# Kernel optimization log

Measured on AMD Instinct MI355X. Metric: run time of the kernel, lower is better.

Reference implementation:

```python
import jax, jax.numpy as jnp
import numpy as np

PD = 256            # pretrain_dim == dim_in (standard mode)
DZ = 128            # dim_z
PD2 = PD + 2        # feature dim after concatenating 2-d coords
FD = PD + 2 * PD2   # final_dim = 772
TEMP = float(DZ) ** 0.5
EPS = 1e-12
N1, N2 = 4096, 2048


def _lin_init(key, din, dout):
    w = jax.random.normal(key, (dout, din), jnp.float32) * 0.02
    b = jnp.zeros((dout,), jnp.float32)
    return w, b


def _lin(x, w, b):
    return x @ w.T + b


def setup_inputs() -> dict:
    key = jax.random.key(0)
    ks = jax.random.split(key, 13)
    lm_X = jax.random.normal(ks[0], (N1, PD), jnp.float32)
    lm_Y = jax.random.normal(ks[1], (N1, 2), jnp.float32)
    tg_X = jax.random.normal(ks[2], (N2, PD), jnp.float32)
    tg_Y = jax.random.normal(ks[3], (N2, 2), jnp.float32)
    lm_delay = jax.random.uniform(ks[4], (N1,), jnp.float32)
    tg_delay = jax.random.uniform(ks[5], (N2,), jnp.float32)
    aq_w, aq_b = _lin_init(ks[6], PD, DZ)    # att_attribute q proj
    ak_w, ak_b = _lin_init(ks[7], PD, DZ)    # att_attribute k proj
    w1_w, w1_b = _lin_init(ks[8], PD2, PD2)  # self.w_1
    w2_w, w2_b = _lin_init(ks[9], PD2, PD2)  # self.w_2
    pq_w, pq_b = _lin_init(ks[10], FD, DZ)   # pred attention q proj
    pk_w, pk_b = _lin_init(ks[11], PD, DZ)   # pred attention k proj
    pv_w, pv_b = _lin_init(ks[12], 2, 2)     # pred attention v proj
    gamma1 = jnp.ones((1, 1), jnp.float32)
    gamma2 = jnp.ones((1, 1), jnp.float32)
    gamma3 = jnp.ones((1, 1), jnp.float32)
    alpha = jnp.ones((1, 1), jnp.float32)
    beta = jnp.zeros((1, 1), jnp.float32)
    return dict(lm_X=lm_X, lm_Y=lm_Y, tg_X=tg_X, tg_Y=tg_Y,
                lm_delay=lm_delay, tg_delay=tg_delay,
                aq_w=aq_w, aq_b=aq_b, ak_w=ak_w, ak_b=ak_b,
                w1_w=w1_w, w1_b=w1_b, w2_w=w2_w, w2_b=w2_b,
                pq_w=pq_w, pq_b=pq_b, pk_w=pk_w, pk_b=pk_b,
                pv_w=pv_w, pv_b=pv_b,
                gamma1=gamma1, gamma2=gamma2, gamma3=gamma3,
                alpha=alpha, beta=beta)


def reference(lm_X, lm_Y, tg_X, tg_Y, lm_delay, tg_delay,
              aq_w, aq_b, ak_w, ak_b,
              w1_w, w1_b, w2_w, w2_b,
              pq_w, pq_b, pk_w, pk_b, pv_w, pv_b,
              gamma1, gamma2, gamma3, alpha, beta):
    n2 = tg_X.shape[0]
    a = alpha[0, 0]
    b0 = beta[0, 0]

    lm_feature = jnp.concatenate([lm_X, lm_Y], axis=1)            # [N1, PD2]
    tg_feature_0 = jnp.concatenate([tg_X, jnp.zeros((n2, 2), lm_X.dtype)], axis=1)
    router_0 = jnp.mean(lm_feature, axis=0)                        # [PD2]

    delay_score = jnp.exp(-gamma1[0, 0] * (a * lm_delay + b0))     # [N1]
    rou0 = jnp.exp(-gamma2[0, 0] * (a * tg_delay + b0))            # [N2]
    rou1 = jnp.exp(-gamma3[0, 0] * (a * tg_delay + b0))            # [N2]

    # SimpleAttention1: attribute score of targets over landmarks
    q = _lin(tg_X, aq_w, aq_b)
    k = _lin(lm_X, ak_w, ak_b)
    attr = jnp.exp(jax.nn.softmax((q / TEMP) @ k.T, axis=-1))      # [N2, N1]

    # Degree-normalized propagation of adj_matrix_0 (block-structured:
    # lm rows = identity, tg rows = [attr | I | rou0-col], router row = [delay | 0 | 1]).
    deg_tg0 = 1.0 + attr.sum(axis=1) + rou0                        # [N2]
    tg_prop0 = (attr @ lm_feature + tg_feature_0 + rou0[:, None] * router_0[None, :]) \
               / (deg_tg0 + EPS)[:, None]
    router_prop0 = (delay_score @ lm_feature + router_0) / (1.0 + delay_score.sum() + EPS)

    tg_feature_1 = _lin(tg_prop0, w1_w, w1_b)                      # [N2, PD2]
    router_1 = _lin(router_prop0[None, :], w1_w, w1_b)             # [1, PD2]

    # Second propagation: adj_matrix_1 = I + rou1 on tg->router column.
    tg_prop1 = (tg_feature_1 + rou1[:, None] * router_1) / (1.0 + rou1 + EPS)[:, None]
    tg_feature_2 = _lin(tg_prop1, w2_w, w2_b)                      # [N2, PD2]

    final_tg_feature = jnp.concatenate([tg_X, tg_feature_1, tg_feature_2], axis=-1)  # [N2, FD]

    # SimpleAttention2 (collaborative MLP prediction)
    q2 = _lin(final_tg_feature, pq_w, pq_b)
    k2 = _lin(lm_X, pk_w, pk_b)
    v2 = _lin(lm_Y, pv_w, pv_b)
    attn2 = jax.nn.softmax((q2 / TEMP) @ k2.T, axis=-1)            # [N2, N1]
    y_pred = attn2 @ v2                                            # [N2, 2]
    return y_pred, final_tg_feature
```

## Files before the change

kernel.cpp:

```cpp
#include <hip/hip_runtime.h>

#define N1 4096
#define N2 2048
#define PD 256
#define DZ 128
#define PD2 258
#define PD2P 264
#define FD 772
#define FDP 776
#define APN 272
#define APLD 72
#define SPLITS 16

typedef short s8v __attribute__((ext_vector_type(8)));
typedef float f32x4 __attribute__((ext_vector_type(4)));

__device__ __forceinline__ short f2b(float f) {
    union { float f; unsigned u; } v; v.f = f;
    unsigned r = v.u + 0x7fffu + ((v.u >> 16) & 1u);
    return (short)(r >> 16);
}
__device__ __forceinline__ float sb2f(short s) {
    union { unsigned u; float f; } v;
    v.u = ((unsigned)(unsigned short)s) << 16;
    return v.f;
}

constexpr int R0 = N2 * PD;
constexpr int R1 = R0 + PD2 * PD2P;
constexpr int R2 = R1 + PD2 * PD2P;
constexpr int R3 = R2 + DZ * FDP;
constexpr int R4 = R3 + APN * N1;
constexpr int R5 = R4 + 4096;
constexpr int R6 = R5 + 2048;
constexpr int R7 = R6 + N2 * 4;
constexpr int R8 = R7 + N2 * 6;

__global__ __launch_bounds__(256) void cvt_all(
    const float* __restrict__ lmX, const float* __restrict__ lmY,
    const float* __restrict__ tgX,
    const float* __restrict__ pqw, const float* __restrict__ w1w,
    const float* __restrict__ w2w,
    const float* __restrict__ lmd, const float* __restrict__ tgd,
    const float* __restrict__ g1, const float* __restrict__ g2,
    const float* __restrict__ g3, const float* __restrict__ al,
    const float* __restrict__ be,
    const float* __restrict__ pvw, const float* __restrict__ pvb,
    short* __restrict__ w1wb, short* __restrict__ w2wb,
    short* __restrict__ pqwb, short* __restrict__ lmFTb,
    float* __restrict__ dscore, float* __restrict__ rou0,
    float* __restrict__ rou1, float* __restrict__ v2b,
    float* __restrict__ Z, short* __restrict__ finalFb,
    short* __restrict__ tgp1b, float* __restrict__ outF)
{
    int i = blockIdx.x * 256 + threadIdx.x;
    if (i < R0) { int r = i >> 8, c = i & 255;
                  float v = tgX[i];
                  outF[(size_t)r * FD + c] = v;
                  finalFb[(size_t)r * FDP + c] = f2b(v); return; }
    if (i < R1) { int j = i - R0; int r = j / PD2P, c = j - r * PD2P;
                  w1wb[j] = (c < PD2) ? f2b(w1w[r * PD2 + c]) : (short)0; return; }
    if (i < R2) { int j = i - R1; int r = j / PD2P, c = j - r * PD2P;
                  w2wb[j] = (c < PD2) ? f2b(w2w[r * PD2 + c]) : (short)0; return; }
    if (i < R3) { int j = i - R2; int r = j / FDP, c = j - r * FDP;
                  pqwb[j] = (c < FD) ? f2b(pqw[r * FD + c]) : (short)0; return; }
    if (i < R4) { int j = i - R3; int c = j >> 12, r = j & (N1 - 1);
                  float v = 0.f;
                  if (c < PD) v = lmX[(size_t)r * PD + c];
                  else if (c < PD2) v = lmY[r * 2 + (c - PD)];
                  else if (c == PD2) v = 1.0f;
                  lmFTb[j] = f2b(v); return; }
    if (i < R5) { int j = i - R4;
                  float a = al[0], b = be[0];
                  dscore[j] = __expf(-g1[0] * (a * lmd[j] + b));
                  float y0 = lmY[2 * j], y1 = lmY[2 * j + 1];
                  v2b[2 * j]     = pvw[0] * y0 + pvw[1] * y1 + pvb[0];
                  v2b[2 * j + 1] = pvw[2] * y0 + pvw[3] * y1 + pvb[1];
                  if (j < N2) { float t = a * tgd[j] + b;
                                rou0[j] = __expf(-g2[0] * t);
                                rou1[j] = __expf(-g3[0] * t); }
                  return; }
    if (i < R6) { Z[i - R5] = 0.f; return; }
    if (i < R7) { int j = i - R6; int r = j >> 2;
                  finalFb[(size_t)r * FDP + FD + (j & 3)] = 0; return; }
    if (i < R8) { int j = i - R7; int r = j / 6;
                  tgp1b[(size_t)r * PD2P + PD2 + (j - r * 6)] = 0; return; }
}

__global__ __launch_bounds__(256) void rkq_kernel(
    const float* __restrict__ lmX, const float* __restrict__ tgX,
    const float* __restrict__ aqw, const float* __restrict__ aqb,
    const float* __restrict__ akw, const float* __restrict__ akb,
    const float* __restrict__ pkw, const float* __restrict__ pkb,
    const short* __restrict__ lmFTb, const float* __restrict__ dscore,
    float* __restrict__ router0, float* __restrict__ routerp0,
    short* __restrict__ kk, short* __restrict__ qb)
{
    __shared__ __align__(16) short LDS[5120];
    const int j = blockIdx.x, tid = threadIdx.x;
    const int lane = tid & 63, wv = tid >> 6;
    const int wm = wv >> 1, wn = wv & 1;
    const int lm = lane & 15, lq = lane >> 4;
    const f32x4 zero4 = {0.f, 0.f, 0.f, 0.f};

    if (j < 258) {
        float* r1 = (float*)LDS;
        float* r2 = r1 + 256;
        float* r3 = r2 + 256;
        const short* rowp = lmFTb + (size_t)j * N1;
        float s1 = 0.f, s2 = 0.f, s3 = 0.f;
        for (int i = tid; i < N1; i += 256) {
            float v = sb2f(rowp[i]);
            float d = dscore[i];
            s1 += v; s2 += d * v; s3 += d;
        }
        r1[tid] = s1; r2[tid] = s2; r3[tid] = s3; __syncthreads();
        for (int o = 128; o > 0; o >>= 1) {
            if (tid < o) { r1[tid] += r1[tid + o]; r2[tid] += r2[tid + o]; r3[tid] += r3[tid + o]; }
            __syncthreads();
        }
        if (tid == 0) {
            float r0v = r1[0] / (float)N1;
            router0[j] = r0v;
            routerp0[j] = (r2[0] + r0v) / (1.f + r3[0] + 1e-12f);
        }
        return;
    }
    short* Als = LDS;
    short* Bls = LDS + 64 * 40;
    f32x4 acc[2][2] = {{zero4, zero4}, {zero4, zero4}};
    const int r = tid >> 2, cgp = tid & 3;
    if (j < 514) {
        int jt = j - 258;
        int row0 = (jt >> 2) * 64, col0 = (jt & 3) * 64;
        for (int k0 = 0; k0 < 256; k0 += 32) {
            int gk = k0 + cgp * 8;
            const float* ap = lmX + (size_t)(row0 + r) * PD + gk;
            int c = col0 + r;
            const float* bp = (c < 128) ? akw + (size_t)c * PD + gk
                                        : pkw + (size_t)(c - 128) * PD + gk;
            s8v va, vb;
#pragma unroll
            for (int q = 0; q < 8; ++q) { va[q] = f2b(ap[q]); vb[q] = f2b(bp[q]); }
            *(s8v*)(Als + r * 40 + cgp * 8) = va;
            *(s8v*)(Bls + r * 40 + cgp * 8) = vb;
            __syncthreads();
            s8v af[2], bf[2];
#pragma unroll
            for (int mt = 0; mt < 2; ++mt)
                af[mt] = *(const s8v*)(Als + (wm * 32 + mt * 16 + lm) * 40 + lq * 8);
#pragma unroll
            for (int nt = 0; nt < 2; ++nt)
                bf[nt] = *(const s8v*)(Bls + (wn * 32 + nt * 16 + lm) * 40 + lq * 8);
#pragma unroll
            for (int mt = 0; mt < 2; ++mt)
#pragma unroll
                for (int nt = 0; nt < 2; ++nt)
                    acc[mt][nt] = __builtin_amdgcn_mfma_f32_16x16x32_bf16(
                        af[mt], bf[nt], acc[mt][nt], 0, 0, 0);
            __syncthreads();
        }
#pragma unroll
        for (int mt = 0; mt < 2; ++mt)
#pragma unroll
            for (int nt = 0; nt < 2; ++nt) {
                int c = col0 + wn * 32 + nt * 16 + lm;
                float bv = (c < 128) ? akb[c] : pkb[c - 128];
#pragma unroll
                for (int i = 0; i < 4; ++i) {
                    int rr = row0 + wm * 32 + mt * 16 + lq * 4 + i;
                    kk[(size_t)rr * 256 + c] = f2b(acc[mt][nt][i] + bv);
                }
            }
    } else {
        int jt = j - 514;
        int row0 = (jt >> 1) * 64, col0 = (jt & 1) * 64;
        for (int k0 = 0; k0 < 256; k0 += 32) {
            int gk = k0 + cgp * 8;
            const float* ap = tgX + (size_t)(row0 + r) * PD + gk;
            const float* bp = aqw + (size_t)(col0 + r) * PD + gk;
            s8v va, vb;
#pragma unroll
            for (int q = 0; q < 8; ++q) { va[q] = f2b(ap[q]); vb[q] = f2b(bp[q]); }
            *(s8v*)(Als + r * 40 + cgp * 8) = va;
            *(s8v*)(Bls + r * 40 + cgp * 8) = vb;
            __syncthreads();
            s8v af[2], bf[2];
#pragma unroll
            for (int mt = 0; mt < 2; ++mt)
                af[mt] = *(const s8v*)(Als + (wm * 32 + mt * 16 + lm) * 40 + lq * 8);
#pragma unroll
            for (int nt = 0; nt < 2; ++nt)
                bf[nt] = *(const s8v*)(Bls + (wn * 32 + nt * 16 + lm) * 40 + lq * 8);
#pragma unroll
            for (int mt = 0; mt < 2; ++mt)
#pragma unroll
                for (int nt = 0; nt < 2; ++nt)
                    acc[mt][nt] = __builtin_amdgcn_mfma_f32_16x16x32_bf16(
                        af[mt], bf[nt], acc[mt][nt], 0, 0, 0);
            __syncthreads();
        }
        const float INV_TEMP = 0.08838834764831845f;
#pragma unroll
        for (int mt = 0; mt < 2; ++mt)
#pragma unroll
            for (int nt = 0; nt < 2; ++nt) {
                int c = col0 + wn * 32 + nt * 16 + lm;
                float bv = aqb[c];
#pragma unroll
                for (int i = 0; i < 4; ++i) {
                    int rr = row0 + wm * 32 + mt * 16 + lq * 4 + i;
                    qb[(size_t)rr * DZ + c] = f2b(INV_TEMP * (acc[mt][nt][i] + bv));
                }
            }
    }
}

__global__ __launch_bounds__(256) void scores_e(
    const short* __restrict__ Q, const short* __restrict__ Kk,
    short* __restrict__ E, float* __restrict__ Z,
    const float* __restrict__ rp0, const float* __restrict__ w1w,
    const float* __restrict__ w1b, float* __restrict__ router1)
{
    const int j = blockIdx.x, tid = threadIdx.x;
    if (j == 512) {
        for (int c = tid; c < PD2; c += 256) {
            float s = w1b[c];
            const float* wr = w1w + (size_t)c * PD2;
            for (int k = 0; k < PD2; ++k) s += rp0[k] * wr[k];
            router1[c] = s;
        }
        return;
    }
    __shared__ __align__(16) short LDS[10240];
    short* Als = LDS;
    short* Bls = LDS + 128 * 40;
    const int lane = tid & 63, wv = tid >> 6;
    const int wm = wv >> 1, wn = wv & 1;
    const int lm = lane & 15, lq = lane >> 4;
    const int row0 = (j >> 5) * 128, col0 = (j & 31) * 128;
    const f32x4 zero4 = {0.f, 0.f, 0.f, 0.f};
    f32x4 acc[4][4];
#pragma unroll
    for (int mt = 0; mt < 4; ++mt)
#pragma unroll
        for (int nt = 0; nt < 4; ++nt) acc[mt][nt] = zero4;
    for (int k0 = 0; k0 < 128; k0 += 32) {
#pragma unroll
        for (int l = 0; l < 2; ++l) {
            int id = l * 256 + tid;
            int r = id >> 2, cgp = id & 3;
            int gk = k0 + cgp * 8;
            *(s8v*)(Als + r * 40 + cgp * 8) = *(const s8v*)(Q + (size_t)(row0 + r) * DZ + gk);
            *(s8v*)(Bls + r * 40 + cgp * 8) = *(const s8v*)(Kk + (size_t)(col0 + r) * 256 + gk);
        }
        __syncthreads();
        s8v af[4], bf[4];
#pragma unroll
        for (int mt = 0; mt < 4; ++mt)
            af[mt] = *(const s8v*)(Als + (wm * 64 + mt * 16 + lm) * 40 + lq * 8);
#pragma unroll
        for (int nt = 0; nt < 4; ++nt)
            bf[nt] = *(const s8v*)(Bls + (wn * 64 + nt * 16 + lm) * 40 + lq * 8);
#pragma unroll
        for (int mt = 0; mt < 4; ++mt)
#pragma unroll
            for (int nt = 0; nt < 4; ++nt)
                acc[mt][nt] = __builtin_amdgcn_mfma_f32_16x16x32_bf16(
                    af[mt], bf[nt], acc[mt][nt], 0, 0, 0);
        __syncthreads();
    }
#pragma unroll
    for (int mt = 0; mt < 4; ++mt)
#pragma unroll
        for (int i = 0; i < 4; ++i) {
            int r = row0 + wm * 64 + mt * 16 + lq * 4 + i;
            float rs = 0.f;
#pragma unroll
            for (int nt = 0; nt < 4; ++nt) {
                int c = col0 + wn * 64 + nt * 16 + lm;
                float e = __expf(acc[mt][nt][i]);
                E[(size_t)r * N1 + c] = f2b(e);
                rs += e;
            }
#pragma unroll
            for (int msk = 1; msk < 16; msk <<= 1) rs += __shfl_xor(rs, msk, 64);
            if (lm == 0) atomicAdd(&Z[r], rs);
        }
}

__global__ __launch_bounds__(512) void ap_gemm(const short* __restrict__ E,
                                               const float* __restrict__ Z,
                                               const short* __restrict__ lmFTb,
                                               short* __restrict__ part)
{
    __shared__ __align__(16) short LDS[28800];
    const int tid = threadIdx.x, bid = blockIdx.x;
    const int lane = tid & 63, w8 = tid >> 6;
    const int lm = lane & 15, lq = lane >> 4;
    const int s = bid & 15, row0 = (bid >> 4) * 128;
    const int kbase = s * (N1 / SPLITS);
    short* Als = LDS;
    short* Bls = LDS + 128 * APLD;
    const f32x4 zero4 = {0.f, 0.f, 0.f, 0.f};
    f32x4 acc[17];
#pragma unroll
    for (int nt = 0; nt < 17; ++nt) acc[nt] = zero4;
    for (int it = 0; it < (N1 / SPLITS) / 64; ++it) {
        int k0 = kbase + it * 64;
#pragma unroll
        for (int l = 0; l < 2; ++l) {
            int id = l * 512 + tid;
            int r = id >> 3, gg = id & 7;
            s8v ev = *(const s8v*)(E + (size_t)(row0 + r) * N1 + k0 + gg * 8);
            float invZ = __builtin_amdgcn_rcpf(Z[row0 + r]);
            s8v av;
#pragma unroll
            for (int q = 0; q < 8; ++q)
                av[q] = f2b(__expf(sb2f(ev[q]) * invZ));
            *(s8v*)(Als + r * APLD + gg * 8) = av;
        }
#pragma unroll
        for (int l = 0; l < 5; ++l) {
            int id = l * 512 + tid;
            if (id < APN * 8) {
                int r = id >> 3, gg = id & 7;
                *(s8v*)(Bls + r * APLD + gg * 8) =
                    *(const s8v*)(lmFTb + (size_t)r * N1 + k0 + gg * 8);
            }
        }
        __syncthreads();
        s8v a0 = *(const s8v*)(Als + (w8 * 16 + lm) * APLD + lq * 8);
        s8v a1 = *(const s8v*)(Als + (w8 * 16 + lm) * APLD + 32 + lq * 8);
#pragma unroll
        for (int nt = 0; nt < 17; ++nt) {
            s8v b0 = *(const s8v*)(Bls + (nt * 16 + lm) * APLD + lq * 8);
            s8v b1 = *(const s8v*)(Bls + (nt * 16 + lm) * APLD + 32 + lq * 8);
            acc[nt] = __builtin_amdgcn_mfma_f32_16x16x32_bf16(a0, b0, acc[nt], 0, 0, 0);
            acc[nt] = __builtin_amdgcn_mfma_f32_16x16x32_bf16(a1, b1, acc[nt], 0, 0, 0);
        }
        __syncthreads();
    }
    short* op = part + (size_t)s * N2 * APN;
#pragma unroll
    for (int nt = 0; nt < 17; ++nt) {
        int c = nt * 16 + lm;
#pragma unroll
        for (int i = 0; i < 4; ++i) {
            int r = row0 + w8 * 16 + lq * 4 + i;
            op[(size_t)r * APN + c] = f2b(acc[nt][i]);
        }
    }
}

__global__ __launch_bounds__(256) void fix_tgp0(const short* __restrict__ part,
                                                const float* __restrict__ tgX,
                                                const float* __restrict__ rou0,
                                                const float* __restrict__ router0,
                                                short* __restrict__ outb) {
    int r = blockIdx.x;
    int tid = threadIdx.x;
    __shared__ float sAsum;
    float s0 = 0.f, s1 = 0.f;
#pragma unroll
    for (int s = 0; s < SPLITS; ++s)
        s0 += sb2f(part[((size_t)s * N2 + r) * APN + tid]);
    if (tid < 8) {
#pragma unroll
        for (int s = 0; s < SPLITS; ++s)
            s1 += sb2f(part[((size_t)s * N2 + r) * APN + 256 + tid]);
    }
    if (tid == 2) sAsum = s1;
    __syncthreads();
    float ro = rou0[r];
    float inv = 1.f / (1.f + sAsum + ro + 1e-12f);
    {
        float v = (s0 + tgX[(size_t)r * PD + tid] + ro * router0[tid]) * inv;
        outb[(size_t)r * PD2P + tid] = f2b(v);
    }
    if (tid < 8) {
        int c = 256 + tid;
        float v = 0.f;
        if (c < PD2) v = (s1 + ro * router0[c]) * inv;
        outb[(size_t)r * PD2P + c] = f2b(v);
    }
}

__global__ __launch_bounds__(256) void w_gemm(
    const short* __restrict__ A, const short* __restrict__ B,
    const float* __restrict__ bias,
    float* __restrict__ outFcol, short* __restrict__ fFbcol,
    const float* __restrict__ rou1, const float* __restrict__ router1,
    short* __restrict__ tgp1b)
{
    __shared__ __align__(16) short LDS[5120];
    short* Als = LDS;
    short* Bls = LDS + 64 * 40;
    const int tid = threadIdx.x;
    const int lane = tid & 63, wv = tid >> 6;
    const int wm = wv >> 1, wn = wv & 1;
    const int lm = lane & 15, lq = lane >> 4;
    const int row0 = blockIdx.y * 64, col0 = blockIdx.x * 64;
    const f32x4 zero4 = {0.f, 0.f, 0.f, 0.f};
    f32x4 acc[2][2] = {{zero4, zero4}, {zero4, zero4}};
    const s8v zero8 = {0, 0, 0, 0, 0, 0, 0, 0};
    const int r = tid >> 2, cgp = tid & 3;
    for (int k0 = 0; k0 < PD2P; k0 += 32) {
        int gk = k0 + cgp * 8;
        s8v va = zero8, vb = zero8;
        if (gk < PD2P) {
            va = *(const s8v*)(A + (size_t)(row0 + r) * PD2P + gk);
            if (col0 + r < PD2) vb = *(const s8v*)(B + (size_t)(col0 + r) * PD2P + gk);
        }
        *(s8v*)(Als + r * 40 + cgp * 8) = va;
        *(s8v*)(Bls + r * 40 + cgp * 8) = vb;
        __syncthreads();
        s8v af[2], bf[2];
#pragma unroll
        for (int mt = 0; mt < 2; ++mt)
            af[mt] = *(const s8v*)(Als + (wm * 32 + mt * 16 + lm) * 40 + lq * 8);
#pragma unroll
        for (int nt = 0; nt < 2; ++nt)
            bf[nt] = *(const s8v*)(Bls + (wn * 32 + nt * 16 + lm) * 40 + lq * 8);
#pragma unroll
        for (int mt = 0; mt < 2; ++mt)
#pragma unroll
            for (int nt = 0; nt < 2; ++nt)
                acc[mt][nt] = __builtin_amdgcn_mfma_f32_16x16x32_bf16(
                    af[mt], bf[nt], acc[mt][nt], 0, 0, 0);
        __syncthreads();
    }
#pragma unroll
    for (int mt = 0; mt < 2; ++mt)
#pragma unroll
        for (int nt = 0; nt < 2; ++nt) {
            int c = col0 + wn * 32 + nt * 16 + lm;
            if (c >= PD2) continue;
            float bv = bias[c];
            float rc = router1 ? router1[c] : 0.f;
#pragma unroll
            for (int i = 0; i < 4; ++i) {
                int rr = row0 + wm * 32 + mt * 16 + lq * 4 + i;
                float v = acc[mt][nt][i] + bv;
                outFcol[(size_t)rr * FD + c] = v;
                fFbcol[(size_t)rr * FDP + c] = f2b(v);
                if (tgp1b) {
                    float ro = rou1[rr];
                    tgp1b[(size_t)rr * PD2P + c] =
                        f2b((v + ro * rc) / (1.f + ro + 1e-12f));
                }
            }
        }
}

__global__ __launch_bounds__(256) void q2_gemm(
    const short* __restrict__ A, const short* __restrict__ B,
    const float* __restrict__ bias, short* __restrict__ outB)
{
    __shared__ __align__(16) short LDS[5120];
    short* Als = LDS;
    short* Bls = LDS + 64 * 40;
    const int tid = threadIdx.x;
    const int lane = tid & 63, wv = tid >> 6;
    const int wm = wv >> 1, wn = wv & 1;
    const int lm = lane & 15, lq = lane >> 4;
    const int row0 = blockIdx.y * 64, col0 = blockIdx.x * 64;
    const f32x4 zero4 = {0.f, 0.f, 0.f, 0.f};
    f32x4 acc[2][2] = {{zero4, zero4}, {zero4, zero4}};
    const s8v zero8 = {0, 0, 0, 0, 0, 0, 0, 0};
    const int r = tid >> 2, cgp = tid & 3;
    for (int k0 = 0; k0 < FDP; k0 += 32) {
        int gk = k0 + cgp * 8;
        s8v va = zero8, vb = zero8;
        if (gk < FDP) {
            va = *(const s8v*)(A + (size_t)(row0 + r) * FDP + gk);
            vb = *(const s8v*)(B + (size_t)(col0 + r) * FDP + gk);
        }
        *(s8v*)(Als + r * 40 + cgp * 8) = va;
        *(s8v*)(Bls + r * 40 + cgp * 8) = vb;
        __syncthreads();
        s8v af[2], bf[2];
#pragma unroll
        for (int mt = 0; mt < 2; ++mt)
            af[mt] = *(const s8v*)(Als + (wm * 32 + mt * 16 + lm) * 40 + lq * 8);
#pragma unroll
        for (int nt = 0; nt < 2; ++nt)
            bf[nt] = *(const s8v*)(Bls + (wn * 32 + nt * 16 + lm) * 40 + lq * 8);
#pragma unroll
        for (int mt = 0; mt < 2; ++mt)
#pragma unroll
            for (int nt = 0; nt < 2; ++nt)
                acc[mt][nt] = __builtin_amdgcn_mfma_f32_16x16x32_bf16(
                    af[mt], bf[nt], acc[mt][nt], 0, 0, 0);
        __syncthreads();
    }
    const float INV_TEMP = 0.08838834764831845f;
#pragma unroll
    for (int mt = 0; mt < 2; ++mt)
#pragma unroll
        for (int nt = 0; nt < 2; ++nt) {
            int c = col0 + wn * 32 + nt * 16 + lm;
            float bv = bias[c];
#pragma unroll
            for (int i = 0; i < 4; ++i) {
                int rr = row0 + wm * 32 + mt * 16 + lq * 4 + i;
                outB[(size_t)rr * DZ + c] = f2b(INV_TEMP * (acc[mt][nt][i] + bv));
            }
        }
}

__global__ __launch_bounds__(256) void attn2_flash(
    const short* __restrict__ Q, const short* __restrict__ Kk,
    const float* __restrict__ V, float* __restrict__ part2)
{
    __shared__ __align__(16) short Qls[64 * 136];
    __shared__ __align__(16) short Kls[64 * 136];
    __shared__ float Vls[128];
    const int tid = threadIdx.x;
    const int lane = tid & 63, wv = tid >> 6;
    const int lm = lane & 15, lq = lane >> 4;
    const int chunk = blockIdx.x & 15, row0 = (blockIdx.x >> 4) * 64;
    const f32x4 zero4 = {0.f, 0.f, 0.f, 0.f};
#pragma unroll
    for (int l = 0; l < 4; ++l) {
        int id = l * 256 + tid;
        int r = id >> 4, g = id & 15;
        *(s8v*)(Qls + r * 136 + g * 8) = *(const s8v*)(Q + (size_t)(row0 + r) * DZ + g * 8);
    }
    __syncthreads();
    s8v af[4];
#pragma unroll
    for (int ks = 0; ks < 4; ++ks)
        af[ks] = *(const s8v*)(Qls + (wv * 16 + lm) * 136 + ks * 32 + lq * 8);
    float z[4] = {0.f, 0.f, 0.f, 0.f};
    float y0[4] = {0.f, 0.f, 0.f, 0.f};
    float y1[4] = {0.f, 0.f, 0.f, 0.f};
    for (int t = 0; t < 4; ++t) {
        int col0 = chunk * 256 + t * 64;
        __syncthreads();
#pragma unroll
        for (int l = 0; l < 4; ++l) {
            int id = l * 256 + tid;
            int r = id >> 4, g = id & 15;
            *(s8v*)(Kls + r * 136 + g * 8) =
                *(const s8v*)(Kk + (size_t)(col0 + r) * 256 + 128 + g * 8);
        }
        if (tid < 128) Vls[tid] = V[col0 * 2 + tid];
        __syncthreads();
        f32x4 acc[4];
#pragma unroll
        for (int nt = 0; nt < 4; ++nt) acc[nt] = zero4;
#pragma unroll
        for (int nt = 0; nt < 4; ++nt)
#pragma unroll
            for (int ks = 0; ks < 4; ++ks) {
                s8v bf = *(const s8v*)(Kls + (nt * 16 + lm) * 136 + ks * 32 + lq * 8);
                acc[nt] = __builtin_amdgcn_mfma_f32_16x16x32_bf16(af[ks], bf, acc[nt], 0, 0, 0);
            }
        float v0[4], v1[4];
#pragma unroll
        for (int nt = 0; nt < 4; ++nt) {
            v0[nt] = Vls[(nt * 16 + lm) * 2];
            v1[nt] = Vls[(nt * 16 + lm) * 2 + 1];
        }
#pragma unroll
        for (int i = 0; i < 4; ++i) {
            float e0 = __expf(acc[0][i]), e1 = __expf(acc[1][i]);
            float e2 = __expf(acc[2][i]), e3 = __expf(acc[3][i]);
            z[i]  += e0 + e1 + e2 + e3;
            y0[i] += e0 * v0[0] + e1 * v0[1] + e2 * v0[2] + e3 * v0[3];
            y1[i] += e0 * v1[0] + e1 * v1[1] + e2 * v1[2] + e3 * v1[3];
        }
    }
#pragma unroll
    for (int i = 0; i < 4; ++i) {
#pragma unroll
        for (int msk = 1; msk < 16; msk <<= 1) {
            z[i]  += __shfl_xor(z[i], msk, 64);
            y0[i] += __shfl_xor(y0[i], msk, 64);
            y1[i] += __shfl_xor(y1[i], msk, 64);
        }
    }
    if (lm == 0) {
#pragma unroll
        for (int i = 0; i < 4; ++i) {
            int r = row0 + wv * 16 + lq * 4 + i;
            float* pp = part2 + ((size_t)r * 16 + chunk) * 4;
            pp[0] = z[i]; pp[1] = y0[i]; pp[2] = y1[i];
        }
    }
}

__global__ void attn2_combine(const float* __restrict__ part2, float* __restrict__ out) {
    int r = blockIdx.x * 256 + threadIdx.x;
    if (r >= N2) return;
    const float* pp = part2 + (size_t)r * 64;
    float Zt = 0.f, Y0 = 0.f, Y1 = 0.f;
#pragma unroll
    for (int c = 0; c < 16; ++c) {
        Zt += pp[c * 4]; Y0 += pp[c * 4 + 1]; Y1 += pp[c * 4 + 2];
    }
    out[2 * r] = Y0 / Zt;
    out[2 * r + 1] = Y1 / Zt;
}

extern "C" void kernel_launch(void* const* d_in, const int* in_sizes, int n_in,
                              void* d_out, int out_size, void* d_ws, size_t ws_size,
                              hipStream_t stream) {
    const float* lm_X = (const float*)d_in[0];
    const float* lm_Y = (const float*)d_in[1];
    const float* tg_X = (const float*)d_in[2];
    const float* lm_delay = (const float*)d_in[4];
    const float* tg_delay = (const float*)d_in[5];
    const float* aq_w = (const float*)d_in[6];
    const float* aq_b = (const float*)d_in[7];
    const float* ak_w = (const float*)d_in[8];
    const float* ak_b = (const float*)d_in[9];
    const float* w1_w = (const float*)d_in[10];
    const float* w1_b = (const float*)d_in[11];
    const float* w2_w = (const float*)d_in[12];
    const float* w2_b = (const float*)d_in[13];
    const float* pq_w = (const float*)d_in[14];
    const float* pq_b = (const float*)d_in[15];
    const float* pk_w = (const float*)d_in[16];
    const float* pk_b = (const float*)d_in[17];
    const float* pv_w = (const float*)d_in[18];
    const float* pv_b = (const float*)d_in[19];
    const float* g1 = (const float*)d_in[20];
    const float* g2 = (const float*)d_in[21];
    const float* g3 = (const float*)d_in[22];
    const float* al = (const float*)d_in[23];
    const float* be = (const float*)d_in[24];

    float* out = (float*)d_out;
    float* outF = out + (size_t)N2 * 2;

    char* base = (char*)d_ws;
    size_t off = 0;
    auto allocF = [&](size_t n) -> float* {
        float* q = (float*)(base + off);
        off += (n * 4 + 255) / 256 * 256;
        return q;
    };
    auto allocS = [&](size_t n) -> short* {
        short* q = (short*)(base + off);
        off += (n * 2 + 255) / 256 * 256;
        return q;
    };

    short* E        = allocS((size_t)N2 * N1);
    short* appart   = allocS((size_t)SPLITS * N2 * APN);
    short* lmFTb    = allocS((size_t)APN * N1);
    short* qb       = allocS((size_t)N2 * DZ);
    short* kk       = allocS((size_t)N1 * 256);
    short* q2       = allocS((size_t)N2 * DZ);
    short* tgp0b    = allocS((size_t)N2 * PD2P);
    short* tgp1b    = allocS((size_t)N2 * PD2P);
    short* finalFb  = allocS((size_t)N2 * FDP);
    short* w1wb     = allocS((size_t)PD2 * PD2P);
    short* w2wb     = allocS((size_t)PD2 * PD2P);
    short* pqwb     = allocS((size_t)DZ * FDP);
    float* v2b      = allocF((size_t)N1 * 2);
    float* part2    = allocF((size_t)N2 * 64);
    float* Zbuf     = allocF(N2);
    float* router0  = allocF(PD2);
    float* routerp0 = allocF(PD2);
    float* router1  = allocF(PD2);
    float* dscore   = allocF(N1);
    float* rou0     = allocF(N2);
    float* rou1     = allocF(N2);

    hipLaunchKernelGGL(cvt_all, dim3((R8 + 255) / 256), dim3(256), 0, stream,
                       lm_X, lm_Y, tg_X, pq_w, w1_w, w2_w,
                       lm_delay, tg_delay, g1, g2, g3, al, be, pv_w, pv_b,
                       w1wb, w2wb, pqwb, lmFTb,
                       dscore, rou0, rou1, v2b, Zbuf, finalFb, tgp1b, outF);
    hipLaunchKernelGGL(rkq_kernel, dim3(578), dim3(256), 0, stream,
                       lm_X, tg_X, aq_w, aq_b, ak_w, ak_b, pk_w, pk_b,
                       lmFTb, dscore, router0, routerp0, kk, qb);
    hipLaunchKernelGGL(scores_e, dim3(513), dim3(256), 0, stream,
                       qb, kk, E, Zbuf, routerp0, w1_w, w1_b, router1);
    hipLaunchKernelGGL(ap_gemm, dim3(256), dim3(512), 0, stream, E, Zbuf, lmFTb, appart);
    hipLaunchKernelGGL(fix_tgp0, dim3(N2), dim3(256), 0, stream,
                       appart, tg_X, rou0, router0, tgp0b);
    hipLaunchKernelGGL(w_gemm, dim3(5, 32), dim3(256), 0, stream,
                       tgp0b, w1wb, w1_b, outF + 256, finalFb + 256, rou1, router1, tgp1b);
    hipLaunchKernelGGL(w_gemm, dim3(5, 32), dim3(256), 0, stream,
                       tgp1b, w2wb, w2_b, outF + 514, finalFb + 514,
                       nullptr, nullptr, nullptr);
    hipLaunchKernelGGL(q2_gemm, dim3(2, 32), dim3(256), 0, stream,
                       finalFb, pqwb, pq_b, q2);
    hipLaunchKernelGGL(attn2_flash, dim3(512), dim3(256), 0, stream,
                       q2, kk, v2b, part2);
    hipLaunchKernelGGL(attn2_combine, dim3(8), dim3(256), 0, stream, part2, out);
}
```

Measured before the change: 217.6 us.

## Fold W2·W1 into one wide GEMM and merge prep kernels with atomic reductions

Precomputes M = W2·W1 in bf16 so tg_feature_2 can be computed directly from tg_prop0 in the same GEMM as tg_feature_1. This removes the second dependent w_gemm launch and the tgp1b intermediate, with router and bias terms folded in algebraically. The conversion kernel and the router/kq kernel are merged into one prep kernel, and the per-column router reductions now use block reductions plus atomics instead of a separate pass. The trade-offs are an extra bf16 rounding of the product matrix, a memset launch, and atomics that make the summation order nondeterministic.

```diff
diff --git a/kernel.cpp b/kernel.cpp
--- a/kernel.cpp
+++ b/kernel.cpp
@@ -26,113 +26,53 @@
     return v.f;
 }
 
-constexpr int R0 = N2 * PD;
-constexpr int R1 = R0 + PD2 * PD2P;
-constexpr int R2 = R1 + PD2 * PD2P;
-constexpr int R3 = R2 + DZ * FDP;
-constexpr int R4 = R3 + APN * N1;
-constexpr int R5 = R4 + 4096;
-constexpr int R6 = R5 + 2048;
-constexpr int R7 = R6 + N2 * 4;
-constexpr int R8 = R7 + N2 * 6;
-
-__global__ __launch_bounds__(256) void cvt_all(
+#define GB_KK  0
+#define GB_QB  256
+#define GB_M   320
+#define GB_FL  345
+constexpr int P0 = 524288;
+constexpr int P1 = P0 + 99328;
+constexpr int P2 = P1 + 1114112;
+constexpr int P3 = P2 + 4096;
+constexpr int P4 = P3 + 8192;
+
+__global__ __launch_bounds__(256) void prep(
     const float* __restrict__ lmX, const float* __restrict__ lmY,
     const float* __restrict__ tgX,
-    const float* __restrict__ pqw, const float* __restrict__ w1w,
-    const float* __restrict__ w2w,
+    const float* __restrict__ aqw, const float* __restrict__ aqb,
+    const float* __restrict__ akw, const float* __restrict__ akb,
+    const float* __restrict__ pkw, const float* __restrict__ pkb,
+    const float* __restrict__ pqw,
+    const float* __restrict__ w1w, const float* __restrict__ w2w,
     const float* __restrict__ lmd, const float* __restrict__ tgd,
     const float* __restrict__ g1, const float* __restrict__ g2,
     const float* __restrict__ g3, const float* __restrict__ al,
     const float* __restrict__ be,
     const float* __restrict__ pvw, const float* __restrict__ pvb,
-    short* __restrict__ w1wb, short* __restrict__ w2wb,
+    float* __restrict__ outF, short* __restrict__ finalFb,
     short* __restrict__ pqwb, short* __restrict__ lmFTb,
-    float* __restrict__ dscore, float* __restrict__ rou0,
-    float* __restrict__ rou1, float* __restrict__ v2b,
-    float* __restrict__ Z, short* __restrict__ finalFb,
-    short* __restrict__ tgp1b, float* __restrict__ outF)
-{
-    int i = blockIdx.x * 256 + threadIdx.x;
-    if (i < R0) { int r = i >> 8, c = i & 255;
-                  float v = tgX[i];
-                  outF[(size_t)r * FD + c] = v;
-                  finalFb[(size_t)r * FDP + c] = f2b(v); return; }
-    if (i < R1) { int j = i - R0; int r = j / PD2P, c = j - r * PD2P;
-                  w1wb[j] = (c < PD2) ? f2b(w1w[r * PD2 + c]) : (short)0; return; }
-    if (i < R2) { int j = i - R1; int r = j / PD2P, c = j - r * PD2P;
-                  w2wb[j] = (c < PD2) ? f2b(w2w[r * PD2 + c]) : (short)0; return; }
-    if (i < R3) { int j = i - R2; int r = j / FDP, c = j - r * FDP;
-                  pqwb[j] = (c < FD) ? f2b(pqw[r * FD + c]) : (short)0; return; }
-    if (i < R4) { int j = i - R3; int c = j >> 12, r = j & (N1 - 1);
-                  float v = 0.f;
-                  if (c < PD) v = lmX[(size_t)r * PD + c];
-                  else if (c < PD2) v = lmY[r * 2 + (c - PD)];
-                  else if (c == PD2) v = 1.0f;
-                  lmFTb[j] = f2b(v); return; }
-    if (i < R5) { int j = i - R4;
-                  float a = al[0], b = be[0];
-                  dscore[j] = __expf(-g1[0] * (a * lmd[j] + b));
-                  float y0 = lmY[2 * j], y1 = lmY[2 * j + 1];
-                  v2b[2 * j]     = pvw[0] * y0 + pvw[1] * y1 + pvb[0];
-                  v2b[2 * j + 1] = pvw[2] * y0 + pvw[3] * y1 + pvb[1];
-                  if (j < N2) { float t = a * tgd[j] + b;
-                                rou0[j] = __expf(-g2[0] * t);
-                                rou1[j] = __expf(-g3[0] * t); }
-                  return; }
-    if (i < R6) { Z[i - R5] = 0.f; return; }
-    if (i < R7) { int j = i - R6; int r = j >> 2;
-                  finalFb[(size_t)r * FDP + FD + (j & 3)] = 0; return; }
-    if (i < R8) { int j = i - R7; int r = j / 6;
-                  tgp1b[(size_t)r * PD2P + PD2 + (j - r * 6)] = 0; return; }
-}
-
-__global__ __launch_bounds__(256) void rkq_kernel(
-    const float* __restrict__ lmX, const float* __restrict__ tgX,
-    const float* __restrict__ aqw, const float* __restrict__ aqb,
-    const float* __restrict__ akw, const float* __restrict__ akb,
-    const float* __restrict__ pkw, const float* __restrict__ pkb,
-    const short* __restrict__ lmFTb, const float* __restrict__ dscore,
-    float* __restrict__ router0, float* __restrict__ routerp0,
-    short* __restrict__ kk, short* __restrict__ qb)
+    float* __restrict__ rou0, float* __restrict__ rou1,
+    float* __restrict__ v2b,
+    float* __restrict__ r0acc, float* __restrict__ rp0acc,
+    float* __restrict__ sumd,
+    short* __restrict__ kk, short* __restrict__ qb,
+    short* __restrict__ Mb)
 {
     __shared__ __align__(16) short LDS[5120];
-    const int j = blockIdx.x, tid = threadIdx.x;
+    const int bid = blockIdx.x, tid = threadIdx.x;
     const int lane = tid & 63, wv = tid >> 6;
     const int wm = wv >> 1, wn = wv & 1;
     const int lm = lane & 15, lq = lane >> 4;
     const f32x4 zero4 = {0.f, 0.f, 0.f, 0.f};
-
-    if (j < 258) {
-        float* r1 = (float*)LDS;
-        float* r2 = r1 + 256;
-        float* r3 = r2 + 256;
-        const short* rowp = lmFTb + (size_t)j * N1;
-        float s1 = 0.f, s2 = 0.f, s3 = 0.f;
-        for (int i = tid; i < N1; i += 256) {
-            float v = sb2f(rowp[i]);
-            float d = dscore[i];
-            s1 += v; s2 += d * v; s3 += d;
-        }
-        r1[tid] = s1; r2[tid] = s2; r3[tid] = s3; __syncthreads();
-        for (int o = 128; o > 0; o >>= 1) {
-            if (tid < o) { r1[tid] += r1[tid + o]; r2[tid] += r2[tid + o]; r3[tid] += r3[tid + o]; }
-            __syncthreads();
-        }
-        if (tid == 0) {
-            float r0v = r1[0] / (float)N1;
-            router0[j] = r0v;
-            routerp0[j] = (r2[0] + r0v) / (1.f + r3[0] + 1e-12f);
-        }
-        return;
-    }
+    const s8v zero8 = {0, 0, 0, 0, 0, 0, 0, 0};
     short* Als = LDS;
     short* Bls = LDS + 64 * 40;
-    f32x4 acc[2][2] = {{zero4, zero4}, {zero4, zero4}};
     const int r = tid >> 2, cgp = tid & 3;
-    if (j < 514) {
-        int jt = j - 258;
+
+    if (bid < GB_QB) {
+        int jt = bid;
         int row0 = (jt >> 2) * 64, col0 = (jt & 3) * 64;
+        f32x4 acc[2][2] = {{zero4, zero4}, {zero4, zero4}};
         for (int k0 = 0; k0 < 256; k0 += 32) {
             int gk = k0 + cgp * 8;
             const float* ap = lmX + (size_t)(row0 + r) * PD + gk;
@@ -172,9 +112,12 @@
                     kk[(size_t)rr * 256 + c] = f2b(acc[mt][nt][i] + bv);
                 }
             }
-    } else {
-        int jt = j - 514;
+        return;
+    }
+    if (bid < GB_M) {
+        int jt = bid - GB_QB;
         int row0 = (jt >> 1) * 64, col0 = (jt & 1) * 64;
+        f32x4 acc[2][2] = {{zero4, zero4}, {zero4, zero4}};
         for (int k0 = 0; k0 < 256; k0 += 32) {
             int gk = k0 + cgp * 8;
             const float* ap = tgX + (size_t)(row0 + r) * PD + gk;
@@ -213,26 +156,163 @@
                     qb[(size_t)rr * DZ + c] = f2b(INV_TEMP * (acc[mt][nt][i] + bv));
                 }
             }
+        return;
+    }
+    if (bid < GB_FL) {
+        int jm = bid - GB_M;
+        int row0 = (jm / 5) * 64, col0 = (jm % 5) * 64;
+        f32x4 acc[2][2] = {{zero4, zero4}, {zero4, zero4}};
+        for (int k0 = 0; k0 < 264; k0 += 32) {
+            int gk = k0 + cgp * 8;
+            s8v va = zero8, vb = zero8;
+            int arow = row0 + r, bcol = col0 + r;
+#pragma unroll
+            for (int q = 0; q < 8; ++q) {
+                int kidx = gk + q;
+                if (kidx < PD2) {
+                    if (arow < PD2) va[q] = f2b(w2w[(size_t)arow * PD2 + kidx]);
+                    if (bcol < PD2) vb[q] = f2b(w1w[(size_t)kidx * PD2 + bcol]);
+                }
+            }
+            *(s8v*)(Als + r * 40 + cgp * 8) = va;
+            *(s8v*)(Bls + r * 40 + cgp * 8) = vb;
+            __syncthreads();
+            s8v af[2], bf[2];
+#pragma unroll
+            for (int mt = 0; mt < 2; ++mt)
+                af[mt] = *(const s8v*)(Als + (wm * 32 + mt * 16 + lm) * 40 + lq * 8);
+#pragma unroll
+            for (int nt = 0; nt < 2; ++nt)
+                bf[nt] = *(const s8v*)(Bls + (wn * 32 + nt * 16 + lm) * 40 + lq * 8);
+#pragma unroll
+            for (int mt = 0; mt < 2; ++mt)
+#pragma unroll
+                for (int nt = 0; nt < 2; ++nt)
+                    acc[mt][nt] = __builtin_amdgcn_mfma_f32_16x16x32_bf16(
+                        af[mt], bf[nt], acc[mt][nt], 0, 0, 0);
+            __syncthreads();
+        }
+#pragma unroll
+        for (int mt = 0; mt < 2; ++mt)
+#pragma unroll
+            for (int nt = 0; nt < 2; ++nt) {
+                int c = col0 + wn * 32 + nt * 16 + lm;
+#pragma unroll
+                for (int i = 0; i < 4; ++i) {
+                    int rr = row0 + wm * 32 + mt * 16 + lq * 4 + i;
+                    if (rr >= PD2 || c >= PD2P) continue;
+                    Mb[(size_t)rr * PD2P + c] = (c < PD2) ? f2b(acc[mt][nt][i]) : (short)0;
+                }
+            }
+        return;
+    }
+    int i = (bid - GB_FL) * 256 + tid;
+    if (i < P0) {
+        int rr = i >> 8, c = i & 255;
+        float v = tgX[i];
+        outF[(size_t)rr * FD + c] = v;
+        finalFb[(size_t)rr * FDP + c] = f2b(v);
+        return;
+    }
+    if (i < P1) {
+        int j = i - P0; int rr = j / FDP, c = j - rr * FDP;
+        pqwb[j] = (c < FD) ? f2b(pqw[(size_t)rr * FD + c]) : (short)0;
+        return;
+    }
+    if (i < P2) {
+        int j = i - P1;
+        int c = j >> 12, rr = j & (N1 - 1);
+        float v = 0.f;
+        if (c < PD) v = lmX[(size_t)rr * PD + c];
+        else if (c < PD2) v = lmY[rr * 2 + (c - PD)];
+        else if (c == PD2) v = 1.0f;
+        lmFTb[j] = f2b(v);
+        if (c < PD2) {
+            float a = al[0], b = be[0];
+            float d = __expf(-g1[0] * (a * lmd[rr] + b));
+            float* red1 = (float*)LDS;
+            float* red2 = red1 + 256;
+            red1[tid] = v; red2[tid] = d * v; __syncthreads();
+            for (int o = 128; o > 0; o >>= 1) {
+                if (tid < o) { red1[tid] += red1[tid + o]; red2[tid] += red2[tid + o]; }
+                __syncthreads();
+            }
+            if (tid == 0) {
+                atomicAdd(&r0acc[c], red1[0]);
+                atomicAdd(&rp0acc[c], red2[0]);
+            }
+        }
+        return;
+    }
+    if (i < P3) {
+        int j = i - P2;
+        float a = al[0], b = be[0];
+        float d = __expf(-g1[0] * (a * lmd[j] + b));
+        float y0 = lmY[2 * j], y1 = lmY[2 * j + 1];
+        v2b[2 * j]     = pvw[0] * y0 + pvw[1] * y1 + pvb[0];
+        v2b[2 * j + 1] = pvw[2] * y0 + pvw[3] * y1 + pvb[1];
+        if (j < N2) {
+            float t = a * tgd[j] + b;
+            rou0[j] = __expf(-g2[0] * t);
+            rou1[j] = __expf(-g3[0] * t);
+        }
+        float* red1 = (float*)LDS;
+        red1[tid] = d; __syncthreads();
+        for (int o = 128; o > 0; o >>= 1) {
+            if (tid < o) red1[tid] += red1[tid + o];
+            __syncthreads();
+        }
+        if (tid == 0) atomicAdd(sumd, red1[0]);
+        return;
+    }
+    {
+        int j = i - P3; int rr = j >> 2;
+        finalFb[(size_t)rr * FDP + FD + (j & 3)] = 0;
     }
 }
 
 __global__ __launch_bounds__(256) void scores_e(
     const short* __restrict__ Q, const short* __restrict__ Kk,
     short* __restrict__ E, float* __restrict__ Z,
-    const float* __restrict__ rp0, const float* __restrict__ w1w,
-    const float* __restrict__ w1b, float* __restrict__ router1)
+    const float* __restrict__ r0acc, const float* __restrict__ rp0acc,
+    const float* __restrict__ sumd,
+    const float* __restrict__ w1w, const float* __restrict__ w1b,
+    const float* __restrict__ w2w,
+    float* __restrict__ router0, float* __restrict__ w2r,
+    float* __restrict__ w2b1)
 {
+    __shared__ __align__(16) short LDS[10240];
     const int j = blockIdx.x, tid = threadIdx.x;
     if (j == 512) {
+        float* rp0l = (float*)LDS;
+        float* r1l = rp0l + 264;
+        float sd = sumd[0];
+        for (int c = tid; c < PD2; c += 256) {
+            float r0v = r0acc[c] * (1.0f / (float)N1);
+            router0[c] = r0v;
+            rp0l[c] = (rp0acc[c] + r0v) / (1.f + sd + 1e-12f);
+        }
+        __syncthreads();
         for (int c = tid; c < PD2; c += 256) {
             float s = w1b[c];
             const float* wr = w1w + (size_t)c * PD2;
-            for (int k = 0; k < PD2; ++k) s += rp0[k] * wr[k];
-            router1[c] = s;
+            for (int k = 0; k < PD2; ++k) s += wr[k] * rp0l[k];
+            r1l[c] = s;
+        }
+        __syncthreads();
+        for (int c = tid; c < PD2; c += 256) {
+            const float* wr = w2w + (size_t)c * PD2;
+            float sr = 0.f, sb = 0.f;
+            for (int k = 0; k < PD2; ++k) {
+                float w = wr[k];
+                sr += w * r1l[k];
+                sb += w * w1b[k];
+            }
+            w2r[c] = sr;
+            w2b1[c] = sb;
         }
         return;
     }
-    __shared__ __align__(16) short LDS[10240];
     short* Als = LDS;
     short* Bls = LDS + 128 * 40;
     const int lane = tid & 63, wv = tid >> 6;
@@ -386,12 +466,13 @@
     }
 }
 
-__global__ __launch_bounds__(256) void w_gemm(
-    const short* __restrict__ A, const short* __restrict__ B,
-    const float* __restrict__ bias,
-    float* __restrict__ outFcol, short* __restrict__ fFbcol,
-    const float* __restrict__ rou1, const float* __restrict__ router1,
-    short* __restrict__ tgp1b)
+__global__ __launch_bounds__(256) void wt_gemm(
+    const short* __restrict__ A, const float* __restrict__ w1w,
+    const short* __restrict__ Mb,
+    const float* __restrict__ w1b, const float* __restrict__ w2b,
+    const float* __restrict__ rou1, const float* __restrict__ w2r,
+    const float* __restrict__ w2b1,
+    float* __restrict__ outF, short* __restrict__ finalFb)
 {
     __shared__ __align__(16) short LDS[5120];
     short* Als = LDS;
@@ -405,12 +486,20 @@
     f32x4 acc[2][2] = {{zero4, zero4}, {zero4, zero4}};
     const s8v zero8 = {0, 0, 0, 0, 0, 0, 0, 0};
     const int r = tid >> 2, cgp = tid & 3;
+    const int j = col0 + r;
     for (int k0 = 0; k0 < PD2P; k0 += 32) {
         int gk = k0 + cgp * 8;
         s8v va = zero8, vb = zero8;
-        if (gk < PD2P) {
+        if (gk < PD2P)
             va = *(const s8v*)(A + (size_t)(row0 + r) * PD2P + gk);
-            if (col0 + r < PD2) vb = *(const s8v*)(B + (size_t)(col0 + r) * PD2P + gk);
+        if (j < PD2) {
+#pragma unroll
+            for (int q = 0; q < 8; ++q) {
+                int kidx = gk + q;
+                if (kidx < PD2) vb[q] = f2b(w1w[(size_t)j * PD2 + kidx]);
+            }
+        } else if (j < 2 * PD2) {
+            if (gk < PD2P) vb = *(const s8v*)(Mb + (size_t)(j - PD2) * PD2P + gk);
         }
         *(s8v*)(Als + r * 40 + cgp * 8) = va;
         *(s8v*)(Bls + r * 40 + cgp * 8) = vb;
@@ -434,21 +523,25 @@
     for (int mt = 0; mt < 2; ++mt)
 #pragma unroll
         for (int nt = 0; nt < 2; ++nt) {
-            int c = col0 + wn * 32 + nt * 16 + lm;
-            if (c >= PD2) continue;
-            float bv = bias[c];
-            float rc = router1 ? router1[c] : 0.f;
+            int jc = col0 + wn * 32 + nt * 16 + lm;
+            if (jc >= 2 * PD2) continue;
 #pragma unroll
             for (int i = 0; i < 4; ++i) {
                 int rr = row0 + wm * 32 + mt * 16 + lq * 4 + i;
-                float v = acc[mt][nt][i] + bv;
-                outFcol[(size_t)rr * FD + c] = v;
-                fFbcol[(size_t)rr * FDP + c] = f2b(v);
-                if (tgp1b) {
+                float v;
+                int oc;
+                if (jc < PD2) {
+                    v = acc[mt][nt][i] + w1b[jc];
+                    oc = 256 + jc;
+                } else {
+                    int c = jc - PD2;
                     float ro = rou1[rr];
-                    tgp1b[(size_t)rr * PD2P + c] =
-                        f2b((v + ro * rc) / (1.f + ro + 1e-12f));
+                    v = (acc[mt][nt][i] + w2b1[c] + ro * w2r[c]) / (1.f + ro + 1e-12f)
+                        + w2b[c];
+                    oc = 514 + c;
                 }
+                outF[(size_t)rr * FD + oc] = v;
+                finalFb[(size_t)rr * FDP + oc] = f2b(v);
             }
         }
 }
@@ -655,39 +748,39 @@
     short* kk       = allocS((size_t)N1 * 256);
     short* q2       = allocS((size_t)N2 * DZ);
     short* tgp0b    = allocS((size_t)N2 * PD2P);
-    short* tgp1b    = allocS((size_t)N2 * PD2P);
     short* finalFb  = allocS((size_t)N2 * FDP);
-    short* w1wb     = allocS((size_t)PD2 * PD2P);
-    short* w2wb     = allocS((size_t)PD2 * PD2P);
     short* pqwb     = allocS((size_t)DZ * FDP);
+    short* Mb       = allocS((size_t)PD2 * PD2P);
     float* v2b      = allocF((size_t)N1 * 2);
     float* part2    = allocF((size_t)N2 * 64);
-    float* Zbuf     = allocF(N2);
-    float* router0  = allocF(PD2);
-    float* routerp0 = allocF(PD2);
-    float* router1  = allocF(PD2);
-    float* dscore   = allocF(N1);
+    float* Zr       = allocF(2048 + 264 + 264 + 8);
+    float* Zbuf     = Zr;
+    float* r0acc    = Zr + 2048;
+    float* rp0acc   = Zr + 2048 + 264;
+    float* sumd     = Zr + 2048 + 528;
+    float* router0  = allocF(264);
+    float* w2r      = allocF(264);
+    float* w2b1     = allocF(264);
     float* rou0     = allocF(N2);
     float* rou1     = allocF(N2);
 
-    hipLaunchKernelGGL(cvt_all, dim3((R8 + 255) / 256), dim3(256), 0, stream,
-                       lm_X, lm_Y, tg_X, pq_w, w1_w, w2_w,
-                       lm_delay, tg_delay, g1, g2, g3, al, be, pv_w, pv_b,
-                       w1wb, w2wb, pqwb, lmFTb,
-                       dscore, rou0, rou1, v2b, Zbuf, finalFb, tgp1b, outF);
-    hipLaunchKernelGGL(rkq_kernel, dim3(578), dim3(256), 0, stream,
-                       lm_X, tg_X, aq_w, aq_b, ak_w, ak_b, pk_w, pk_b,
-                       lmFTb, dscore, router0, routerp0, kk, qb);
+    hipMemsetAsync(Zr, 0, (2048 + 264 + 264 + 8) * sizeof(float), stream);
+
+    hipLaunchKernelGGL(prep, dim3(GB_FL + P4 / 256), dim3(256), 0, stream,
+                       lm_X, lm_Y, tg_X, aq_w, aq_b, ak_w, ak_b, pk_w, pk_b,
+                       pq_w, w1_w, w2_w, lm_delay, tg_delay,
+                       g1, g2, g3, al, be, pv_w, pv_b,
+                       outF, finalFb, pqwb, lmFTb, rou0, rou1, v2b,
+                       r0acc, rp0acc, sumd, kk, qb, Mb);
     hipLaunchKernelGGL(scores_e, dim3(513), dim3(256), 0, stream,
-                       qb, kk, E, Zbuf, routerp0, w1_w, w1_b, router1);
+                       qb, kk, E, Zbuf, r0acc, rp0acc, sumd,
+                       w1_w, w1_b, w2_w, router0, w2r, w2b1);
     hipLaunchKernelGGL(ap_gemm, dim3(256), dim3(512), 0, stream, E, Zbuf, lmFTb, appart);
     hipLaunchKernelGGL(fix_tgp0, dim3(N2), dim3(256), 0, stream,
                        appart, tg_X, rou0, router0, tgp0b);
-    hipLaunchKernelGGL(w_gemm, dim3(5, 32), dim3(256), 0, stream,
-                       tgp0b, w1wb, w1_b, outF + 256, finalFb + 256, rou1, router1, tgp1b);
-    hipLaunchKernelGGL(w_gemm, dim3(5, 32), dim3(256), 0, stream,
-                       tgp1b, w2wb, w2_b, outF + 514, finalFb + 514,
-                       nullptr, nullptr, nullptr);
+    hipLaunchKernelGGL(wt_gemm, dim3(9, 32), dim3(256), 0, stream,
+                       tgp0b, w1_w, Mb, w1_b, w2_b, rou1, w2r, w2b1,
+                       outF, finalFb);
     hipLaunchKernelGGL(q2_gemm, dim3(2, 32), dim3(256), 0, stream,
                        finalFb, pqwb, pq_b, q2);
     hipLaunchKernelGGL(attn2_flash, dim3(512), dim3(256), 0, stream,
```

After: 266.4 us. 22.4% more time.
